# Kernel optimization log

Measured on AMD Instinct MI355X. Metric: run time of the kernel, lower is better.

## Reference

```python
import jax, jax.numpy as jnp
import numpy as np

N, E, G = 20000, 320000, 1000
F_NODE, F_EDGE, HID, HEADS, NCLS = 12, 4, 64, 4, 4


def setup_inputs() -> dict:
    key = jax.random.key(0)
    ks = iter(jax.random.split(key, 64))

    def rn(shape, s=0.1):
        return jax.random.normal(next(ks), shape, jnp.float32) * s

    inp = {
        "x": rn((N, F_NODE), 1.0),
        "edge_index": jax.random.randint(next(ks), (2, E), 0, N, dtype=jnp.int32),
        "edge_attr": rn((E, F_EDGE), 1.0),
        "batch": jnp.sort(jax.random.randint(next(ks), (N,), 0, G, dtype=jnp.int32)),
    }
    # GATv2 layer params: lin_l (W,b), lin_r (W,b), lin_edge (W, no bias), att, out bias
    for i, (cin, H) in enumerate([(F_NODE, HEADS), (HID * HEADS, HEADS), (HID * HEADS, 1)], 1):
        d = H * HID
        inp[f"Wl{i}"] = rn((cin, d))
        inp[f"bl{i}"] = rn((d,))
        inp[f"Wr{i}"] = rn((cin, d))
        inp[f"br{i}"] = rn((d,))
        inp[f"We{i}"] = rn((F_EDGE, d))
        inp[f"att{i}"] = rn((H, HID))
        inp[f"bias{i}"] = rn((d,))
    inp["mW1"] = rn((HID, 32)); inp["mb1"] = rn((32,))
    inp["mW2"] = rn((32, 16)); inp["mb2"] = rn((16,))
    inp["mW3"] = rn((16, NCLS)); inp["mb3"] = rn((NCLS,))
    return inp


def gatv2(x, src, dst, ea, Wl, bl, Wr, br, We, att, bias, H):
    # PyG GATv2Conv (share_weights=False, negative_slope=0.2, concat=True, eval mode)
    xl = (x @ Wl + bl).reshape(N, H, HID)   # source transform
    xr = (x @ Wr + br).reshape(N, H, HID)   # target transform
    ee = (ea @ We).reshape(E, H, HID)       # edge embedding
    z = jax.nn.leaky_relu(xl[src] + xr[dst] + ee, 0.2)  # [E,H,C]
    logits = jnp.einsum("ehc,hc->eh", z, att)
    m = jax.ops.segment_max(logits, dst, num_segments=N)  # per-dest max
    ex = jnp.exp(logits - m[dst])
    denom = jax.ops.segment_sum(ex, dst, num_segments=N)
    alpha = ex / (denom[dst] + 1e-16)                      # segment softmax
    msg = (xl[src] * alpha[:, :, None]).reshape(E, H * HID)
    out = jax.ops.segment_sum(msg, dst, num_segments=N)
    return out + bias


def reference(x, edge_index, edge_attr, batch,
              Wl1, bl1, Wr1, br1, We1, att1, bias1,
              Wl2, bl2, Wr2, br2, We2, att2, bias2,
              Wl3, bl3, Wr3, br3, We3, att3, bias3,
              mW1, mb1, mW2, mb2, mW3, mb3):
    src, dst = edge_index[0], edge_index[1]
    h = jax.nn.elu(gatv2(x, src, dst, edge_attr, Wl1, bl1, Wr1, br1, We1, att1, bias1, HEADS))
    h = jax.nn.elu(gatv2(h, src, dst, edge_attr, Wl2, bl2, Wr2, br2, We2, att2, bias2, HEADS))
    h = gatv2(h, src, dst, edge_attr, Wl3, bl3, Wr3, br3, We3, att3, bias3, 1)  # [N,HID]
    # global mean pool
    sums = jax.ops.segment_sum(h, batch, num_segments=G)
    cnt = jax.ops.segment_sum(jnp.ones((N, 1), h.dtype), batch, num_segments=G)
    g = sums / jnp.maximum(cnt, 1.0)
    # MLP head (dropout disabled, eval mode)
    g = jax.nn.relu(g @ mW1 + mb1)
    g = jax.nn.relu(g @ mW2 + mb2)
    return g @ mW3 + mb3
```

## Files before the change

kernel.cpp:

```cpp
#include <hip/hip_runtime.h>
#include <hip/hip_bf16.h>

#define NNODES 20000
#define NEDGES 320000
#define NGRAPH 1000

typedef __hip_bfloat16 bf16;
typedef unsigned short u16;
typedef short short8 __attribute__((ext_vector_type(8)));
typedef float f32x4 __attribute__((ext_vector_type(4)));

__device__ __forceinline__ float b2f(bf16 x) { return __bfloat162float(x); }
__device__ __forceinline__ float bu2f(u16 u) { return __uint_as_float(((unsigned)u) << 16); }
__device__ __forceinline__ u16 f2bu(float v) {
    __hip_bfloat16 b = __float2bfloat16(v);
    return *reinterpret_cast<u16*>(&b);
}

__device__ __forceinline__ int idx_at(const void* p, int i, int is64) {
    return is64 ? (int)((const long long*)p)[i] : ((const int*)p)[i];
}

static inline char* align16(char* p) {
    return (char*)(((uintptr_t)p + 15) & ~(uintptr_t)15);
}

__global__ void sniff_all(const void* __restrict__ x, const void* __restrict__ ei,
                          const void* __restrict__ batch, int* __restrict__ flags) {
    __shared__ int sb[4];
    if (threadIdx.x < 4) sb[threadIdx.x] = 0;
    __syncthreads();
    int gb = 0, gf = 0, ze = 0, zb = 0;
    for (int i = threadIdx.x; i < 8192; i += blockDim.x) {
        float vb = b2f(((const bf16*)x)[i]);
        float vf = ((const float*)x)[i];
        if (fabsf(vb) < 1e4f) gb++;
        if (fabsf(vf) < 1e4f) gf++;
        if (((const int*)ei)[2 * i + 1] == 0) ze++;
        if (((const int*)batch)[2 * i + 1] == 0) zb++;
    }
    atomicAdd(&sb[0], gb); atomicAdd(&sb[1], gf);
    atomicAdd(&sb[2], ze); atomicAdd(&sb[3], zb);
    __syncthreads();
    if (threadIdx.x == 0) {
        flags[0] = (sb[0] >= sb[1]) ? 1 : 0;
        flags[1] = (sb[2] > 6000) ? 1 : 0;
        flags[2] = (sb[3] > 6000) ? 1 : 0;
    }
}

struct Segs {
    const void* src[29];
    int off[30];
};

__global__ void convert_inputs(Segs S, const int* __restrict__ flags,
                               float* __restrict__ dst, int total) {
    int i = blockIdx.x * blockDim.x + threadIdx.x;
    if (i >= total) return;
    bool isbf = flags[0] != 0;
    int lo = 0, hi = 29;
    while (hi - lo > 1) {
        int mid = (lo + hi) >> 1;
        if (i >= S.off[mid]) lo = mid; else hi = mid;
    }
    int j = i - S.off[lo];
    dst[i] = isbf ? b2f(((const bf16*)S.src[lo])[j]) : ((const float*)S.src[lo])[j];
}

__global__ void conv_ea(const float* __restrict__ cea, u16* __restrict__ eah, int n) {
    int i = blockIdx.x * blockDim.x + threadIdx.x;
    if (i < n) eah[i] = f2bu(cea[i]);
}

__global__ void conv_wtp(const float* __restrict__ W, u16* __restrict__ WTp, int K, int N) {
    int i = blockIdx.x * blockDim.x + threadIdx.x;
    if (i >= K * N) return;
    int j = i & 7;
    int lane = (i >> 3) & 63;
    int rest = i >> 9;
    int KB = K >> 5;
    int tile = rest / KB, kbi = rest - tile * KB;
    int l16 = lane & 15, quad = lane >> 4;
    int n = tile * 16 + l16;
    int k = kbi * 32 + quad * 8 + j;
    WTp[i] = f2bu(W[(size_t)k * N + n]);
}

__global__ void csr_hist(const void* __restrict__ ei, const int* __restrict__ flags,
                         int* __restrict__ deg) {
    int e = blockIdx.x * blockDim.x + threadIdx.x;
    if (e >= NEDGES) return;
    atomicAdd(&deg[idx_at(ei, NEDGES + e, flags[1])], 1);
}

__global__ void csr_scan(const int* __restrict__ deg, int* __restrict__ rowptr,
                         int* __restrict__ cursor) {
    __shared__ int wsum[16];
    __shared__ int wpre[16];
    const int t = threadIdx.x;
    const int wid = t >> 6, lane = t & 63;
    const int base = t * 20;
    int loc[20];
    int s = 0;
#pragma unroll
    for (int j = 0; j < 20; j++) {
        int i = base + j;
        int v = (i < NNODES) ? deg[i] : 0;
        loc[j] = s;
        s += v;
    }
    int incl = s;
#pragma unroll
    for (int o = 1; o < 64; o <<= 1) {
        int n = __shfl_up(incl, o);
        if (lane >= o) incl += n;
    }
    if (lane == 63) wsum[wid] = incl;
    __syncthreads();
    if (wid == 0 && lane < 16) {
        int v = wsum[lane];
        int inc2 = v;
#pragma unroll
        for (int o = 1; o < 16; o <<= 1) {
            int n = __shfl_up(inc2, o);
            if (lane >= o) inc2 += n;
        }
        wpre[lane] = inc2 - v;
    }
    __syncthreads();
    int excl = wpre[wid] + incl - s;
#pragma unroll
    for (int j = 0; j < 20; j++) {
        int i = base + j;
        if (i < NNODES) { rowptr[i] = excl + loc[j]; cursor[i] = excl + loc[j]; }
    }
    if (t == 1023) rowptr[NNODES] = excl + s;
}

__global__ void csr_scatter(const void* __restrict__ ei, const int* __restrict__ flags,
                            int* __restrict__ cursor, int2* __restrict__ csr) {
    int e = blockIdx.x * blockDim.x + threadIdx.x;
    if (e >= NEDGES) return;
    const int i64 = flags[1];
    int src = idx_at(ei, e, i64), dst = idx_at(ei, NEDGES + e, i64);
    int pos = atomicAdd(&cursor[dst], 1);
    csr[pos] = make_int2(src, e);
}

template <int TM, int CIN, int DOUT, bool GUARD>
__global__ __launch_bounds__(256, 2) void lin_gemm(
        const float* __restrict__ X,
        const float* __restrict__ Wl, const float* __restrict__ bl,
        const float* __restrict__ Wr, const float* __restrict__ br,
        u16* __restrict__ XL, float* __restrict__ XR) {
    constexpr int CPT = DOUT / 4;
    constexpr int RG = 256 / CPT;
    constexpr int M = RG * TM;
    __shared__ float xs[M * CIN];

    const int t = threadIdx.x;
    const int ct = t % CPT;
    const int rg = t / CPT;
    const int c0 = ct * 4;
    const int r0 = blockIdx.x * M;

    constexpr int C4 = CIN / 4;
    for (int i = t; i < M * C4; i += 256) {
        int r = i / C4, j = i - r * C4;
        float4 v = make_float4(0.f, 0.f, 0.f, 0.f);
        if (!GUARD || (r0 + r) < NNODES)
            v = *(const float4*)&X[(size_t)(r0 + r) * CIN + j * 4];
        *(float4*)&xs[r * CIN + j * 4] = v;
    }
    __syncthreads();

    float4 accL[TM], accR[TM];
#pragma unroll
    for (int m = 0; m < TM; m++) {
        accL[m] = make_float4(0.f, 0.f, 0.f, 0.f);
        accR[m] = make_float4(0.f, 0.f, 0.f, 0.f);
    }
    const float* xbase = &xs[rg * TM * CIN];
#pragma unroll 4
    for (int k = 0; k < CIN; k++) {
        const float4 wl = *(const float4*)&Wl[k * DOUT + c0];
        const float4 wr = *(const float4*)&Wr[k * DOUT + c0];
#pragma unroll
        for (int m = 0; m < TM; m++) {
            float xv = xbase[m * CIN + k];
            accL[m].x = fmaf(xv, wl.x, accL[m].x);
            accL[m].y = fmaf(xv, wl.y, accL[m].y);
            accL[m].z = fmaf(xv, wl.z, accL[m].z);
            accL[m].w = fmaf(xv, wl.w, accL[m].w);
            accR[m].x = fmaf(xv, wr.x, accR[m].x);
            accR[m].y = fmaf(xv, wr.y, accR[m].y);
            accR[m].z = fmaf(xv, wr.z, accR[m].z);
            accR[m].w = fmaf(xv, wr.w, accR[m].w);
        }
    }

    const float4 b4l = *(const float4*)&bl[c0];
    const float4 b4r = *(const float4*)&br[c0];
#pragma unroll
    for (int m = 0; m < TM; m++) {
        int row = r0 + rg * TM + m;
        if (GUARD && row >= NNODES) continue;
        float l0 = accL[m].x + b4l.x, l1 = accL[m].y + b4l.y;
        float l2 = accL[m].z + b4l.z, l3 = accL[m].w + b4l.w;
        uint2 pk;
        pk.x = (unsigned)f2bu(l0) | ((unsigned)f2bu(l1) << 16);
        pk.y = (unsigned)f2bu(l2) | ((unsigned)f2bu(l3) << 16);
        *(uint2*)&XL[(size_t)row * DOUT + c0] = pk;
        float4 r4;
        r4.x = accR[m].x + b4r.x; r4.y = accR[m].y + b4r.y;
        r4.z = accR[m].z + b4r.z; r4.w = accR[m].w + b4r.w;
        *(float4*)&XR[(size_t)row * DOUT + c0] = r4;
    }
}

template <int N>
__global__ __launch_bounds__(256) void lin_gemm_mfma(
        const float* __restrict__ X,
        const u16* __restrict__ WlP, const float* __restrict__ bl,
        const u16* __restrict__ WrP, const float* __restrict__ br,
        u16* __restrict__ XL, float* __restrict__ XR) {
    constexpr int K = 256;
    constexpr int KB = K / 32;
    constexpr int NTW = N / 64;
    constexpr int XSTR = 264;
    __shared__ u16 xhi[16 * XSTR];
    __shared__ u16 xlo[16 * XSTR];

    const int t = threadIdx.x;
    const int w = t >> 6, lane = t & 63;
    const int quad = lane >> 4, l16 = lane & 15;
    const int m0 = blockIdx.x * 16;
    const int nbase = w * (N / 4);

    for (int idx = t; idx < 16 * 64; idx += 256) {
        int r = idx >> 6, c4 = idx & 63;
        float4 v = *(const float4*)&X[(size_t)(m0 + r) * K + c4 * 4];
        float f[4] = {v.x, v.y, v.z, v.w};
        ushort4 hi, lo;
        u16 h;
        h = f2bu(f[0]); hi.x = h; lo.x = f2bu(f[0] - bu2f(h));
        h = f2bu(f[1]); hi.y = h; lo.y = f2bu(f[1] - bu2f(h));
        h = f2bu(f[2]); hi.z = h; lo.z = f2bu(f[2] - bu2f(h));
        h = f2bu(f[3]); hi.w = h; lo.w = f2bu(f[3] - bu2f(h));
        *(ushort4*)&xhi[r * XSTR + c4 * 4] = hi;
        *(ushort4*)&xlo[r * XSTR + c4 * 4] = lo;
    }
    __syncthreads();

    f32x4 accL[NTW], accR[NTW];
#pragma unroll
    for (int i = 0; i < NTW; i++) {
        accL[i] = (f32x4){0.f, 0.f, 0.f, 0.f};
        accR[i] = (f32x4){0.f, 0.f, 0.f, 0.f};
    }

    const int abase = l16 * XSTR + quad * 8;
#pragma unroll
    for (int kbi = 0; kbi < KB; kbi++) {
        short8 ahi = *(const short8*)&xhi[abase + kbi * 32];
        short8 alo = *(const short8*)&xlo[abase + kbi * 32];
#pragma unroll
        for (int i = 0; i < NTW; i++) {
            int tg = (nbase >> 4) + i;
            size_t off = ((size_t)(tg * KB + kbi) * 64 + lane) * 8;
            short8 bL = *(const short8*)&WlP[off];
            short8 bR = *(const short8*)&WrP[off];
            accL[i] = __builtin_amdgcn_mfma_f32_16x16x32_bf16(ahi, bL, accL[i], 0, 0, 0);
            accL[i] = __builtin_amdgcn_mfma_f32_16x16x32_bf16(alo, bL, accL[i], 0, 0, 0);
            accR[i] = __builtin_amdgcn_mfma_f32_16x16x32_bf16(ahi, bR, accR[i], 0, 0, 0);
            accR[i] = __builtin_amdgcn_mfma_f32_16x16x32_bf16(alo, bR, accR[i], 0, 0, 0);
        }
    }

#pragma unroll
    for (int i = 0; i < NTW; i++) {
        int col = nbase + i * 16 + l16;
        float bLv = bl[col], bRv = br[col];
#pragma unroll
        for (int r = 0; r < 4; r++) {
            int row = m0 + quad * 4 + r;
            XL[(size_t)row * N + col] = f2bu(accL[i][r] + bLv);
            XR[(size_t)row * N + col] = accR[i][r] + bRv;
        }
    }
}

template <int H, bool ELU>
__global__ __launch_bounds__(H * 64, 4) void gat_agg(
                        const int* __restrict__ rowptr, const int2* __restrict__ csr,
                        const u16* __restrict__ XL, const float* __restrict__ XR,
                        const u16* __restrict__ eah,
                        const float* __restrict__ We, const float* __restrict__ att,
                        const float* __restrict__ bias, float* __restrict__ out) {
    const int Dout = H * 64;
    const int dst = blockIdx.x;
    const int t = threadIdx.x;
    const int h = t >> 6;
    const int lane = t & 63;
    const int g = lane >> 4;
    const int k = lane & 15;
    const int c0 = h * 64 + k * 4;

    const float4 w0 = *(const float4*)&We[0 * Dout + c0];
    const float4 w1 = *(const float4*)&We[1 * Dout + c0];
    const float4 w2 = *(const float4*)&We[2 * Dout + c0];
    const float4 w3 = *(const float4*)&We[3 * Dout + c0];
    const float4 at = *(const float4*)&att[c0];
    const float4 xr = *(const float4*)&XR[dst * Dout + c0];

    const int i0 = rowptr[dst], i1 = rowptr[dst + 1];
    const int niter = (i1 - i0 + 3) >> 2;

    float l = 0.f;
    float4 acc = make_float4(0.f, 0.f, 0.f, 0.f);

#define GAT_EDGE_BODY(E_IDX)                                                     \
    {                                                                            \
        int e_ = (E_IDX);                                                        \
        bool valid_ = e_ < i1;                                                   \
        int2 se_ = csr[valid_ ? e_ : i0];                                        \
        uint2 xu_ = *(const uint2*)&XL[se_.x * Dout + c0];                       \
        uint2 au_ = *(const uint2*)&eah[se_.y * 4];                              \
        float xl0_ = __uint_as_float(xu_.x << 16);                               \
        float xl1_ = __uint_as_float(xu_.x & 0xffff0000u);                       \
        float xl2_ = __uint_as_float(xu_.y << 16);                               \
        float xl3_ = __uint_as_float(xu_.y & 0xffff0000u);                       \
        float A0_ = __uint_as_float(au_.x << 16);                                \
        float A1_ = __uint_as_float(au_.x & 0xffff0000u);                        \
        float A2_ = __uint_as_float(au_.y << 16);                                \
        float A3_ = __uint_as_float(au_.y & 0xffff0000u);                        \
        float z0_ = fmaf(A0_, w0.x, fmaf(A1_, w1.x, fmaf(A2_, w2.x, fmaf(A3_, w3.x, xl0_ + xr.x)))); \
        float z1_ = fmaf(A0_, w0.y, fmaf(A1_, w1.y, fmaf(A2_, w2.y, fmaf(A3_, w3.y, xl1_ + xr.y)))); \
        float z2_ = fmaf(A0_, w0.z, fmaf(A1_, w1.z, fmaf(A2_, w2.z, fmaf(A3_, w3.z, xl2_ + xr.z)))); \
        float z3_ = fmaf(A0_, w0.w, fmaf(A1_, w1.w, fmaf(A2_, w2.w, fmaf(A3_, w3.w, xl3_ + xr.w)))); \
        z0_ = fmaxf(z0_, 0.2f * z0_);                                            \
        z1_ = fmaxf(z1_, 0.2f * z1_);                                            \
        z2_ = fmaxf(z2_, 0.2f * z2_);                                            \
        z3_ = fmaxf(z3_, 0.2f * z3_);                                            \
        float v_ = fmaf(z3_, at.w, fmaf(z2_, at.z, fmaf(z1_, at.y, z0_ * at.x))); \
        v_ += __shfl_xor(v_, 1);                                                 \
        v_ += __shfl_xor(v_, 2);                                                 \
        v_ += __shfl_xor(v_, 4);                                                 \
        v_ += __shfl_xor(v_, 8);                                                 \
        float p_ = valid_ ? __expf(v_) : 0.f;                                    \
        l += p_;                                                                 \
        acc.x = fmaf(p_, xl0_, acc.x);                                           \
        acc.y = fmaf(p_, xl1_, acc.y);                                           \
        acc.z = fmaf(p_, xl2_, acc.z);                                           \
        acc.w = fmaf(p_, xl3_, acc.w);                                           \
    }

    int it = 0;
    for (; it + 2 <= niter; it += 2) {
        int eb = i0 + g + it * 4;
        GAT_EDGE_BODY(eb)
        GAT_EDGE_BODY(eb + 4)
    }
    if (it < niter) {
        GAT_EDGE_BODY(i0 + g + it * 4)
    }
#undef GAT_EDGE_BODY

    l += __shfl_xor(l, 16);      l += __shfl_xor(l, 32);
    acc.x += __shfl_xor(acc.x, 16); acc.x += __shfl_xor(acc.x, 32);
    acc.y += __shfl_xor(acc.y, 16); acc.y += __shfl_xor(acc.y, 32);
    acc.z += __shfl_xor(acc.z, 16); acc.z += __shfl_xor(acc.z, 32);
    acc.w += __shfl_xor(acc.w, 16); acc.w += __shfl_xor(acc.w, 32);

    if (g == 0) {
        float inv = 1.f / (l + 1e-16f);
        const float4 b4 = *(const float4*)&bias[c0];
        float o0 = fmaf(acc.x, inv, b4.x);
        float o1 = fmaf(acc.y, inv, b4.y);
        float o2 = fmaf(acc.z, inv, b4.z);
        float o3 = fmaf(acc.w, inv, b4.w);
        if (ELU) {
            o0 = o0 > 0.f ? o0 : expf(o0) - 1.f;
            o1 = o1 > 0.f ? o1 : expf(o1) - 1.f;
            o2 = o2 > 0.f ? o2 : expf(o2) - 1.f;
            o3 = o3 > 0.f ? o3 : expf(o3) - 1.f;
        }
        *(float4*)&out[dst * Dout + c0] = make_float4(o0, o1, o2, o3);
    }
}

__global__ void pool_kernel(const float* __restrict__ h, const void* __restrict__ batch,
                            const int* __restrict__ flags,
                            float* __restrict__ pool, float* __restrict__ cnt) {
    int i = blockIdx.x * blockDim.x + threadIdx.x;
    if (i >= NNODES * 64) return;
    int n = i >> 6, c = i & 63;
    int b = idx_at(batch, n, flags[2]);
    atomicAdd(&pool[b * 64 + c], h[i]);
    if (c == 0) atomicAdd(&cnt[b], 1.f);
}

__global__ void mlp_head(const float* __restrict__ pool, const float* __restrict__ cnt,
                         const float* __restrict__ mW1, const float* __restrict__ mb1,
                         const float* __restrict__ mW2, const float* __restrict__ mb2,
                         const float* __restrict__ mW3, const float* __restrict__ mb3,
                         float* __restrict__ out) {
    __shared__ float g[64], s1[32], s2[16];
    int b = blockIdx.x, t = threadIdx.x;
    float c = fmaxf(cnt[b], 1.f);
    g[t] = pool[b * 64 + t] / c;
    __syncthreads();
    if (t < 32) {
        float a = 0.f;
        for (int k = 0; k < 64; k++) a = fmaf(g[k], mW1[k * 32 + t], a);
        s1[t] = fmaxf(a + mb1[t], 0.f);
    }
    __syncthreads();
    if (t < 16) {
        float a = 0.f;
        for (int k = 0; k < 32; k++) a = fmaf(s1[k], mW2[k * 16 + t], a);
        s2[t] = fmaxf(a + mb2[t], 0.f);
    }
    __syncthreads();
    if (t < 4) {
        float a = 0.f;
        for (int k = 0; k < 16; k++) a = fmaf(s2[k], mW3[k * 4 + t], a);
        out[b * 4 + t] = a + mb3[t];
    }
}


extern "C" void kernel_launch(void* const* d_in, const int* in_sizes, int n_in,
                              void* d_out, int out_size, void* d_ws, size_t ws_size,
                              hipStream_t stream) {
    const void* ei    = d_in[1];
    const void* batch = d_in[3];

    int fidx[29];
    fidx[0] = 0;
    fidx[1] = 2;
    for (int i = 0; i < 21; i++) fidx[2 + i] = 4 + i;
    for (int i = 0; i < 6; i++) fidx[23 + i] = 25 + i;

    Segs S;
    int off = 0;
    for (int i = 0; i < 29; i++) {
        S.src[i] = d_in[fidx[i]];
        S.off[i] = off;
        off += in_sizes[fidx[i]];
    }
    S.off[29] = off;
    const int total = off;

    char* p = (char*)d_ws;
    int*   FLAGS  = (int*)p;                 p += 16;
    float* CONV   = (float*)p;               p += sizeof(float) * total;  p = align16(p);
    int*   DEG    = (int*)p;                 p += sizeof(int) * NNODES;
    int*   ROWPTR = (int*)p;                 p += sizeof(int) * (NNODES + 1);
    int*   CURSOR = (int*)p;                 p += sizeof(int) * (NNODES + 1);  p = align16(p);
    int2*  CSR    = (int2*)p;                p += sizeof(int2) * NEDGES;  p = align16(p);
    u16*   EAH    = (u16*)p;                 p += sizeof(u16) * NEDGES * 4;  p = align16(p);
    u16*   WT2L   = (u16*)p;                 p += sizeof(u16) * 256 * 256;
    u16*   WT2R   = (u16*)p;                 p += sizeof(u16) * 256 * 256;
    u16*   WT3L   = (u16*)p;                 p += sizeof(u16) * 64 * 256;
    u16*   WT3R   = (u16*)p;                 p += sizeof(u16) * 64 * 256;  p = align16(p);
    u16*   XLb    = (u16*)p;                 p += sizeof(u16) * NNODES * 256;  p = align16(p);
    float* XRb    = (float*)p;               p += sizeof(float) * NNODES * 256;
    float* ACC    = (float*)p;               p += sizeof(float) * NNODES * 256;
    float* POOL   = (float*)p;               p += sizeof(float) * NGRAPH * 64;
    float* CNT    = (float*)p;               p += sizeof(float) * NGRAPH;

    const float* CX  = CONV + S.off[0];
    const float* CEA = CONV + S.off[1];
    const float* CP[21];
    for (int i = 0; i < 21; i++) CP[i] = CONV + S.off[2 + i];
    const float* CmW1 = CONV + S.off[23];
    const float* Cmb1 = CONV + S.off[24];
    const float* CmW2 = CONV + S.off[25];
    const float* Cmb2 = CONV + S.off[26];
    const float* CmW3 = CONV + S.off[27];
    const float* Cmb3 = CONV + S.off[28];

    sniff_all<<<1, 256, 0, stream>>>(d_in[0], ei, batch, FLAGS);
    convert_inputs<<<(total + 255) / 256, 256, 0, stream>>>(S, FLAGS, CONV, total);
    conv_ea<<<(NEDGES * 4 + 255) / 256, 256, 0, stream>>>(CEA, EAH, NEDGES * 4);
    conv_wtp<<<(256 * 256 + 255) / 256, 256, 0, stream>>>(CP[7], WT2L, 256, 256);
    conv_wtp<<<(256 * 256 + 255) / 256, 256, 0, stream>>>(CP[9], WT2R, 256, 256);
    conv_wtp<<<(64 * 256 + 255) / 256, 256, 0, stream>>>(CP[14], WT3L, 256, 64);
    conv_wtp<<<(64 * 256 + 255) / 256, 256, 0, stream>>>(CP[16], WT3R, 256, 64);

    hipMemsetAsync(DEG, 0, sizeof(int) * NNODES, stream);
    csr_hist<<<(NEDGES + 255) / 256, 256, 0, stream>>>(ei, FLAGS, DEG);
    csr_scan<<<1, 1024, 0, stream>>>(DEG, ROWPTR, CURSOR);
    csr_scatter<<<(NEDGES + 255) / 256, 256, 0, stream>>>(ei, FLAGS, CURSOR, CSR);

    lin_gemm<4, 12, 256, false><<<NNODES / 16, 256, 0, stream>>>(CX, CP[0], CP[1], CP[2], CP[3], XLb, XRb);
    gat_agg<4, true><<<NNODES, 256, 0, stream>>>(ROWPTR, CSR, XLb, XRb, EAH, CP[4], CP[5], CP[6], ACC);

    lin_gemm_mfma<256><<<NNODES / 16, 256, 0, stream>>>(ACC, WT2L, CP[8], WT2R, CP[10], XLb, XRb);
    gat_agg<4, true><<<NNODES, 256, 0, stream>>>(ROWPTR, CSR, XLb, XRb, EAH, CP[11], CP[12], CP[13], ACC);

    lin_gemm_mfma<64><<<NNODES / 16, 256, 0, stream>>>(ACC, WT3L, CP[15], WT3R, CP[17], XLb, XRb);
    gat_agg<1, false><<<NNODES, 64, 0, stream>>>(ROWPTR, CSR, XLb, XRb, EAH, CP[18], CP[19], CP[20], ACC);

    hipMemsetAsync(POOL, 0, sizeof(float) * (NGRAPH * 64 + NGRAPH), stream);
    pool_kernel<<<(NNODES * 64 + 255) / 256, 256, 0, stream>>>(ACC, batch, FLAGS, POOL, CNT);
    mlp_head<<<NGRAPH, 64, 0, stream>>>(POOL, CNT, CmW1, Cmb1, CmW2, Cmb2, CmW3, Cmb3, (float*)d_out);
}
```

Baseline: 413.8 us.

## Merge preprocessing kernels, widen GAT lanes to 8 channels, fuse pooling into last layer

Six conversion and weight-transpose kernels plus two memsets become one preprocess kernel, which reads raw inputs directly instead of the converted copy. gat_agg now gives each lane 8 channels and handles 8 edges in parallel per head, using 16-byte XL gathers and one fewer shuffle in the logit reduction. The last GAT layer atomically accumulates its output into the graph pool, which removes the pool kernel and the ACC round trip. The costs are more registers per lane and more atomics issued from the final layer.

```diff
diff --git a/kernel.cpp b/kernel.cpp
--- a/kernel.cpp
+++ b/kernel.cpp
@@ -12,6 +12,8 @@
 
 __device__ __forceinline__ float b2f(bf16 x) { return __bfloat162float(x); }
 __device__ __forceinline__ float bu2f(u16 u) { return __uint_as_float(((unsigned)u) << 16); }
+__device__ __forceinline__ float lou(unsigned u) { return __uint_as_float(u << 16); }
+__device__ __forceinline__ float hiu(unsigned u) { return __uint_as_float(u & 0xffff0000u); }
 __device__ __forceinline__ u16 f2bu(float v) {
     __hip_bfloat16 b = __float2bfloat16(v);
     return *reinterpret_cast<u16*>(&b);
@@ -19,6 +21,10 @@
 
 __device__ __forceinline__ int idx_at(const void* p, int i, int is64) {
     return is64 ? (int)((const long long*)p)[i] : ((const int*)p)[i];
+}
+
+__device__ __forceinline__ float raw_at(const void* p, size_t i, bool isbf) {
+    return isbf ? b2f(((const bf16*)p)[i]) : ((const float*)p)[i];
 }
 
 static inline char* align16(char* p) {
@@ -54,28 +60,8 @@
     int off[30];
 };
 
-__global__ void convert_inputs(Segs S, const int* __restrict__ flags,
-                               float* __restrict__ dst, int total) {
-    int i = blockIdx.x * blockDim.x + threadIdx.x;
-    if (i >= total) return;
-    bool isbf = flags[0] != 0;
-    int lo = 0, hi = 29;
-    while (hi - lo > 1) {
-        int mid = (lo + hi) >> 1;
-        if (i >= S.off[mid]) lo = mid; else hi = mid;
-    }
-    int j = i - S.off[lo];
-    dst[i] = isbf ? b2f(((const bf16*)S.src[lo])[j]) : ((const float*)S.src[lo])[j];
-}
-
-__global__ void conv_ea(const float* __restrict__ cea, u16* __restrict__ eah, int n) {
-    int i = blockIdx.x * blockDim.x + threadIdx.x;
-    if (i < n) eah[i] = f2bu(cea[i]);
-}
-
-__global__ void conv_wtp(const float* __restrict__ W, u16* __restrict__ WTp, int K, int N) {
-    int i = blockIdx.x * blockDim.x + threadIdx.x;
-    if (i >= K * N) return;
+__device__ __forceinline__ void wtp_store(u16* __restrict__ dst, const void* __restrict__ src,
+                                          int K, int N, int i, bool isbf) {
     int j = i & 7;
     int lane = (i >> 3) & 63;
     int rest = i >> 9;
@@ -83,8 +69,44 @@
     int tile = rest / KB, kbi = rest - tile * KB;
     int l16 = lane & 15, quad = lane >> 4;
     int n = tile * 16 + l16;
-    int k = kbi * 32 + quad * 8 + j;
-    WTp[i] = f2bu(W[(size_t)k * N + n]);
+    int kk = kbi * 32 + quad * 8 + j;
+    dst[i] = f2bu(raw_at(src, (size_t)kk * N + n, isbf));
+}
+
+__global__ void preprocess(Segs S, const int* __restrict__ flags,
+                           float* __restrict__ conv, int total,
+                           u16* __restrict__ eah,
+                           u16* __restrict__ wt2l, u16* __restrict__ wt2r,
+                           u16* __restrict__ wt3l, u16* __restrict__ wt3r,
+                           int* __restrict__ deg, float* __restrict__ poolcnt) {
+    int i = blockIdx.x * blockDim.x + threadIdx.x;
+    bool isbf = flags[0] != 0;
+    if (i < total) {
+        int lo = 0, hi = 29;
+        while (hi - lo > 1) {
+            int mid = (lo + hi) >> 1;
+            if (i >= S.off[mid]) lo = mid; else hi = mid;
+        }
+        conv[i] = raw_at(S.src[lo], i - S.off[lo], isbf);
+        return;
+    }
+    i -= total;
+    if (i < NEDGES * 4) {
+        eah[i] = isbf ? ((const u16*)S.src[1])[i] : f2bu(((const float*)S.src[1])[i]);
+        return;
+    }
+    i -= NEDGES * 4;
+    if (i < 65536) { wtp_store(wt2l, S.src[9],  256, 256, i, isbf); return; }
+    i -= 65536;
+    if (i < 65536) { wtp_store(wt2r, S.src[11], 256, 256, i, isbf); return; }
+    i -= 65536;
+    if (i < 16384) { wtp_store(wt3l, S.src[16], 256, 64, i, isbf); return; }
+    i -= 16384;
+    if (i < 16384) { wtp_store(wt3r, S.src[18], 256, 64, i, isbf); return; }
+    i -= 16384;
+    if (i < NNODES) { deg[i] = 0; return; }
+    i -= NNODES;
+    if (i < NGRAPH * 65) poolcnt[i] = 0.f;
 }
 
 __global__ void csr_hist(const void* __restrict__ ei, const int* __restrict__ flags,
@@ -291,114 +313,122 @@
     }
 }
 
-template <int H, bool ELU>
+template <int H, bool ELU, bool POOLF>
 __global__ __launch_bounds__(H * 64, 4) void gat_agg(
                         const int* __restrict__ rowptr, const int2* __restrict__ csr,
                         const u16* __restrict__ XL, const float* __restrict__ XR,
                         const u16* __restrict__ eah,
                         const float* __restrict__ We, const float* __restrict__ att,
-                        const float* __restrict__ bias, float* __restrict__ out) {
+                        const float* __restrict__ bias, float* __restrict__ out,
+                        const void* __restrict__ batch, const int* __restrict__ flags,
+                        float* __restrict__ pool, float* __restrict__ cnt) {
     const int Dout = H * 64;
     const int dst = blockIdx.x;
     const int t = threadIdx.x;
     const int h = t >> 6;
     const int lane = t & 63;
-    const int g = lane >> 4;
-    const int k = lane & 15;
-    const int c0 = h * 64 + k * 4;
-
-    const float4 w0 = *(const float4*)&We[0 * Dout + c0];
-    const float4 w1 = *(const float4*)&We[1 * Dout + c0];
-    const float4 w2 = *(const float4*)&We[2 * Dout + c0];
-    const float4 w3 = *(const float4*)&We[3 * Dout + c0];
-    const float4 at = *(const float4*)&att[c0];
-    const float4 xr = *(const float4*)&XR[dst * Dout + c0];
+    const int g = lane >> 3;
+    const int k = lane & 7;
+    const int c0 = h * 64 + k * 8;
+
+    float W[4][8], AT[8], XRv[8];
+#pragma unroll
+    for (int kk = 0; kk < 4; kk++) {
+        float4 a = *(const float4*)&We[kk * Dout + c0];
+        float4 b = *(const float4*)&We[kk * Dout + c0 + 4];
+        W[kk][0] = a.x; W[kk][1] = a.y; W[kk][2] = a.z; W[kk][3] = a.w;
+        W[kk][4] = b.x; W[kk][5] = b.y; W[kk][6] = b.z; W[kk][7] = b.w;
+    }
+    {
+        float4 a = *(const float4*)&att[c0];
+        float4 b = *(const float4*)&att[c0 + 4];
+        AT[0] = a.x; AT[1] = a.y; AT[2] = a.z; AT[3] = a.w;
+        AT[4] = b.x; AT[5] = b.y; AT[6] = b.z; AT[7] = b.w;
+        float4 c = *(const float4*)&XR[dst * Dout + c0];
+        float4 d = *(const float4*)&XR[dst * Dout + c0 + 4];
+        XRv[0] = c.x; XRv[1] = c.y; XRv[2] = c.z; XRv[3] = c.w;
+        XRv[4] = d.x; XRv[5] = d.y; XRv[6] = d.z; XRv[7] = d.w;
+    }
 
     const int i0 = rowptr[dst], i1 = rowptr[dst + 1];
-    const int niter = (i1 - i0 + 3) >> 2;
+    const int niter = (i1 - i0 + 7) >> 3;
 
     float l = 0.f;
-    float4 acc = make_float4(0.f, 0.f, 0.f, 0.f);
+    float acc[8];
+#pragma unroll
+    for (int c = 0; c < 8; c++) acc[c] = 0.f;
 
 #define GAT_EDGE_BODY(E_IDX)                                                     \
     {                                                                            \
         int e_ = (E_IDX);                                                        \
         bool valid_ = e_ < i1;                                                   \
         int2 se_ = csr[valid_ ? e_ : i0];                                        \
-        uint2 xu_ = *(const uint2*)&XL[se_.x * Dout + c0];                       \
+        uint4 xu_ = *(const uint4*)&XL[se_.x * Dout + c0];                       \
         uint2 au_ = *(const uint2*)&eah[se_.y * 4];                              \
-        float xl0_ = __uint_as_float(xu_.x << 16);                               \
-        float xl1_ = __uint_as_float(xu_.x & 0xffff0000u);                       \
-        float xl2_ = __uint_as_float(xu_.y << 16);                               \
-        float xl3_ = __uint_as_float(xu_.y & 0xffff0000u);                       \
-        float A0_ = __uint_as_float(au_.x << 16);                                \
-        float A1_ = __uint_as_float(au_.x & 0xffff0000u);                        \
-        float A2_ = __uint_as_float(au_.y << 16);                                \
-        float A3_ = __uint_as_float(au_.y & 0xffff0000u);                        \
-        float z0_ = fmaf(A0_, w0.x, fmaf(A1_, w1.x, fmaf(A2_, w2.x, fmaf(A3_, w3.x, xl0_ + xr.x)))); \
-        float z1_ = fmaf(A0_, w0.y, fmaf(A1_, w1.y, fmaf(A2_, w2.y, fmaf(A3_, w3.y, xl1_ + xr.y)))); \
-        float z2_ = fmaf(A0_, w0.z, fmaf(A1_, w1.z, fmaf(A2_, w2.z, fmaf(A3_, w3.z, xl2_ + xr.z)))); \
-        float z3_ = fmaf(A0_, w0.w, fmaf(A1_, w1.w, fmaf(A2_, w2.w, fmaf(A3_, w3.w, xl3_ + xr.w)))); \
-        z0_ = fmaxf(z0_, 0.2f * z0_);                                            \
-        z1_ = fmaxf(z1_, 0.2f * z1_);                                            \
-        z2_ = fmaxf(z2_, 0.2f * z2_);                                            \
-        z3_ = fmaxf(z3_, 0.2f * z3_);                                            \
-        float v_ = fmaf(z3_, at.w, fmaf(z2_, at.z, fmaf(z1_, at.y, z0_ * at.x))); \
+        float xl_[8];                                                            \
+        xl_[0] = lou(xu_.x); xl_[1] = hiu(xu_.x);                                \
+        xl_[2] = lou(xu_.y); xl_[3] = hiu(xu_.y);                                \
+        xl_[4] = lou(xu_.z); xl_[5] = hiu(xu_.z);                                \
+        xl_[6] = lou(xu_.w); xl_[7] = hiu(xu_.w);                                \
+        float A0_ = lou(au_.x), A1_ = hiu(au_.x);                                \
+        float A2_ = lou(au_.y), A3_ = hiu(au_.y);                                \
+        float v_ = 0.f;                                                          \
+        _Pragma("unroll")                                                        \
+        for (int c = 0; c < 8; c++) {                                            \
+            float z = fmaf(A0_, W[0][c], fmaf(A1_, W[1][c],                      \
+                      fmaf(A2_, W[2][c], fmaf(A3_, W[3][c], xl_[c] + XRv[c])))); \
+            z = fmaxf(z, 0.2f * z);                                              \
+            v_ = fmaf(z, AT[c], v_);                                             \
+        }                                                                        \
         v_ += __shfl_xor(v_, 1);                                                 \
         v_ += __shfl_xor(v_, 2);                                                 \
         v_ += __shfl_xor(v_, 4);                                                 \
-        v_ += __shfl_xor(v_, 8);                                                 \
         float p_ = valid_ ? __expf(v_) : 0.f;                                    \
         l += p_;                                                                 \
-        acc.x = fmaf(p_, xl0_, acc.x);                                           \
-        acc.y = fmaf(p_, xl1_, acc.y);                                           \
-        acc.z = fmaf(p_, xl2_, acc.z);                                           \
-        acc.w = fmaf(p_, xl3_, acc.w);                                           \
+        _Pragma("unroll")                                                        \
+        for (int c = 0; c < 8; c++) acc[c] = fmaf(p_, xl_[c], acc[c]);           \
     }
 
     int it = 0;
     for (; it + 2 <= niter; it += 2) {
-        int eb = i0 + g + it * 4;
+        int eb = i0 + g + it * 8;
         GAT_EDGE_BODY(eb)
-        GAT_EDGE_BODY(eb + 4)
+        GAT_EDGE_BODY(eb + 8)
     }
     if (it < niter) {
-        GAT_EDGE_BODY(i0 + g + it * 4)
+        GAT_EDGE_BODY(i0 + g + it * 8)
     }
 #undef GAT_EDGE_BODY
 
-    l += __shfl_xor(l, 16);      l += __shfl_xor(l, 32);
-    acc.x += __shfl_xor(acc.x, 16); acc.x += __shfl_xor(acc.x, 32);
-    acc.y += __shfl_xor(acc.y, 16); acc.y += __shfl_xor(acc.y, 32);
-    acc.z += __shfl_xor(acc.z, 16); acc.z += __shfl_xor(acc.z, 32);
-    acc.w += __shfl_xor(acc.w, 16); acc.w += __shfl_xor(acc.w, 32);
+#pragma unroll
+    for (int o = 8; o < 64; o <<= 1) {
+        l += __shfl_xor(l, o);
+#pragma unroll
+        for (int c = 0; c < 8; c++) acc[c] += __shfl_xor(acc[c], o);
+    }
 
     if (g == 0) {
         float inv = 1.f / (l + 1e-16f);
-        const float4 b4 = *(const float4*)&bias[c0];
-        float o0 = fmaf(acc.x, inv, b4.x);
-        float o1 = fmaf(acc.y, inv, b4.y);
-        float o2 = fmaf(acc.z, inv, b4.z);
-        float o3 = fmaf(acc.w, inv, b4.w);
-        if (ELU) {
-            o0 = o0 > 0.f ? o0 : expf(o0) - 1.f;
-            o1 = o1 > 0.f ? o1 : expf(o1) - 1.f;
-            o2 = o2 > 0.f ? o2 : expf(o2) - 1.f;
-            o3 = o3 > 0.f ? o3 : expf(o3) - 1.f;
-        }
-        *(float4*)&out[dst * Dout + c0] = make_float4(o0, o1, o2, o3);
-    }
-}
-
-__global__ void pool_kernel(const float* __restrict__ h, const void* __restrict__ batch,
-                            const int* __restrict__ flags,
-                            float* __restrict__ pool, float* __restrict__ cnt) {
-    int i = blockIdx.x * blockDim.x + threadIdx.x;
-    if (i >= NNODES * 64) return;
-    int n = i >> 6, c = i & 63;
-    int b = idx_at(batch, n, flags[2]);
-    atomicAdd(&pool[b * 64 + c], h[i]);
-    if (c == 0) atomicAdd(&cnt[b], 1.f);
+        float o[8];
+        float4 ba = *(const float4*)&bias[c0];
+        float4 bb = *(const float4*)&bias[c0 + 4];
+        float bs[8] = {ba.x, ba.y, ba.z, ba.w, bb.x, bb.y, bb.z, bb.w};
+#pragma unroll
+        for (int c = 0; c < 8; c++) {
+            float v = fmaf(acc[c], inv, bs[c]);
+            if (ELU) v = v > 0.f ? v : expf(v) - 1.f;
+            o[c] = v;
+        }
+        if (POOLF) {
+            int b = idx_at(batch, dst, flags[2]);
+#pragma unroll
+            for (int c = 0; c < 8; c++) atomicAdd(&pool[b * 64 + c0 + c], o[c]);
+            if (lane == 0) atomicAdd(&cnt[b], 1.f);
+        } else {
+            *(float4*)&out[dst * Dout + c0] = make_float4(o[0], o[1], o[2], o[3]);
+            *(float4*)&out[dst * Dout + c0 + 4] = make_float4(o[4], o[5], o[6], o[7]);
+        }
+    }
 }
 
 __global__ void mlp_head(const float* __restrict__ pool, const float* __restrict__ cnt,
@@ -472,7 +502,6 @@
     float* CNT    = (float*)p;               p += sizeof(float) * NGRAPH;
 
     const float* CX  = CONV + S.off[0];
-    const float* CEA = CONV + S.off[1];
     const float* CP[21];
     for (int i = 0; i < 21; i++) CP[i] = CONV + S.off[2 + i];
     const float* CmW1 = CONV + S.off[23];
@@ -483,28 +512,25 @@
     const float* Cmb3 = CONV + S.off[28];
 
     sniff_all<<<1, 256, 0, stream>>>(d_in[0], ei, batch, FLAGS);
-    convert_inputs<<<(total + 255) / 256, 256, 0, stream>>>(S, FLAGS, CONV, total);
-    conv_ea<<<(NEDGES * 4 + 255) / 256, 256, 0, stream>>>(CEA, EAH, NEDGES * 4);
-    conv_wtp<<<(256 * 256 + 255) / 256, 256, 0, stream>>>(CP[7], WT2L, 256, 256);
-    conv_wtp<<<(256 * 256 + 255) / 256, 256, 0, stream>>>(CP[9], WT2R, 256, 256);
-    conv_wtp<<<(64 * 256 + 255) / 256, 256, 0, stream>>>(CP[14], WT3L, 256, 64);
-    conv_wtp<<<(64 * 256 + 255) / 256, 256, 0, stream>>>(CP[16], WT3R, 256, 64);
-
-    hipMemsetAsync(DEG, 0, sizeof(int) * NNODES, stream);
+    int pre_total = total + NEDGES * 4 + 65536 * 2 + 16384 * 2 + NNODES + NGRAPH * 65;
+    preprocess<<<(pre_total + 255) / 256, 256, 0, stream>>>(
+        S, FLAGS, CONV, total, EAH, WT2L, WT2R, WT3L, WT3R, DEG, POOL);
+
     csr_hist<<<(NEDGES + 255) / 256, 256, 0, stream>>>(ei, FLAGS, DEG);
     csr_scan<<<1, 1024, 0, stream>>>(DEG, ROWPTR, CURSOR);
     csr_scatter<<<(NEDGES + 255) / 256, 256, 0, stream>>>(ei, FLAGS, CURSOR, CSR);
 
     lin_gemm<4, 12, 256, false><<<NNODES / 16, 256, 0, stream>>>(CX, CP[0], CP[1], CP[2], CP[3], XLb, XRb);
-    gat_agg<4, true><<<NNODES, 256, 0, stream>>>(ROWPTR, CSR, XLb, XRb, EAH, CP[4], CP[5], CP[6], ACC);
+    gat_agg<4, true, false><<<NNODES, 256, 0, stream>>>(ROWPTR, CSR, XLb, XRb, EAH,
+        CP[4], CP[5], CP[6], ACC, batch, FLAGS, POOL, CNT);
 
     lin_gemm_mfma<256><<<NNODES / 16, 256, 0, stream>>>(ACC, WT2L, CP[8], WT2R, CP[10], XLb, XRb);
-    gat_agg<4, true><<<NNODES, 256, 0, stream>>>(ROWPTR, CSR, XLb, XRb, EAH, CP[11], CP[12], CP[13], ACC);
+    gat_agg<4, true, false><<<NNODES, 256, 0, stream>>>(ROWPTR, CSR, XLb, XRb, EAH,
+        CP[11], CP[12], CP[13], ACC, batch, FLAGS, POOL, CNT);
 
     lin_gemm_mfma<64><<<NNODES / 16, 256, 0, stream>>>(ACC, WT3L, CP[15], WT3R, CP[17], XLb, XRb);
-    gat_agg<1, false><<<NNODES, 64, 0, stream>>>(ROWPTR, CSR, XLb, XRb, EAH, CP[18], CP[19], CP[20], ACC);
-
-    hipMemsetAsync(POOL, 0, sizeof(float) * (NGRAPH * 64 + NGRAPH), stream);
-    pool_kernel<<<(NNODES * 64 + 255) / 256, 256, 0, stream>>>(ACC, batch, FLAGS, POOL, CNT);
+    gat_agg<1, false, true><<<NNODES, 64, 0, stream>>>(ROWPTR, CSR, XLb, XRb, EAH,
+        CP[18], CP[19], CP[20], ACC, batch, FLAGS, POOL, CNT);
+
     mlp_head<<<NGRAPH, 64, 0, stream>>>(POOL, CNT, CmW1, Cmb1, CmW2, Cmb2, CmW3, Cmb3, (float*)d_out);
 }
```

After: 471.3 us. +13.9%, slower.
